# Optimization experiments

Hardware: AMD Instinct MI355X
Metric: run time of the kernel (lower is better)

## Reference

```python
import jax, jax.numpy as jnp
import numpy as np

B, L, D, H = 4, 1024, 1024, 16
HD = D // H
SCALE = 1.0 / np.sqrt(HD)
NOISE_PROB = 0.05
NOISE_SCALE = 0.1


def _linear(x, w, b):
    # torch nn.Linear convention: y = x @ W^T + b, W: [out, in]
    return x @ w.T + b


def _quantum_noise(key, real, imag, p=NOISE_PROB, s=NOISE_SCALE):
    """Phase flips, amplitude noise, and measurement dropout on a complex
    tensor represented as (real, imag). Deterministic given `key`."""
    k_phase, k_amp, k_nr, k_ni, k_meas = jax.random.split(key, 5)
    shape = real.shape
    flip = jnp.where(jax.random.uniform(k_phase, shape) < p, -1.0, 1.0)
    amp_mask = (jax.random.uniform(k_amp, shape) < p).astype(real.dtype)
    new_r = real * flip + jax.random.normal(k_nr, shape, real.dtype) * s * amp_mask
    new_i = imag * flip + jax.random.normal(k_ni, shape, imag.dtype) * s * amp_mask
    keep = 1.0 - (jax.random.uniform(k_meas, shape) < p * 0.5).astype(real.dtype)
    return new_r * keep, new_i * keep


def _heads(t):
    # [B, L, D] -> [B, H, L, HD]
    b, l, _ = t.shape
    return t.reshape(b, l, H, HD).transpose(0, 2, 1, 3)


def setup_inputs() -> dict:
    key = jax.random.key(0)
    ks = jax.random.split(key, 16)
    inp = {
        "x_real": jax.random.normal(ks[0], (B, L, D), jnp.float32),
        "x_imag": jax.random.normal(ks[1], (B, L, D), jnp.float32),
        "mask": jnp.ones((B, L), jnp.int32),
    }
    names = ["qr", "qi", "kr", "ki", "vr", "vi", "or", "oi"]
    for i, n in enumerate(names):
        inp[n + "_w"] = jax.random.normal(ks[2 + i], (D, D), jnp.float32) * 0.02
        inp[n + "_b"] = jnp.zeros((D,), jnp.float32)
    ent = jnp.eye(H) + (jax.random.normal(ks[10], (H, H)) * 0.1) * (
        jax.random.uniform(ks[11], (H, H)) < 0.2
    ).astype(jnp.float32)
    inp["ent"] = ent
    return inp


def reference(x_real, x_imag, mask, qr_w, qr_b, qi_w, qi_b, kr_w, kr_b,
              ki_w, ki_b, vr_w, vr_b, vi_w, vi_b, or_w, or_b, oi_w, oi_b, ent):
    # complex Q/K/V: real part from x.real, imag part from x.imag
    q_r, q_i = _linear(x_real, qr_w, qr_b), _linear(x_imag, qi_w, qi_b)
    k_r, k_i = _linear(x_real, kr_w, kr_b), _linear(x_imag, ki_w, ki_b)
    v_r, v_i = _linear(x_real, vr_w, vr_b), _linear(x_imag, vi_w, vi_b)

    nkey = jax.random.key(1)
    q_r, q_i = _quantum_noise(jax.random.fold_in(nkey, 0), q_r, q_i)
    k_r, k_i = _quantum_noise(jax.random.fold_in(nkey, 1), k_r, k_i)
    v_r, v_i = _quantum_noise(jax.random.fold_in(nkey, 2), v_r, v_i)

    q_r, q_i, k_r, k_i, v_r, v_i = map(_heads, (q_r, q_i, k_r, k_i, v_r, v_i))

    # torch.einsum('bhld,hh->bhld') == per-head scaling by diag(ent)
    d = jnp.diagonal(ent)[None, :, None, None]
    q_r, q_i = q_r * d, q_i * d
    k_r, k_i = k_r * d, k_i * d

    # Re(q . conj(k)) interference score: [B, H, Lq, Lk]
    scores = (jnp.einsum("bhqd,bhkd->bhqk", q_r, k_r)
              + jnp.einsum("bhqd,bhkd->bhqk", q_i, k_i)) * SCALE
    scores = jnp.where(mask[:, None, None, :] == 0, -1e9, scores)
    attn = jax.nn.softmax(scores, axis=-1)

    out_r = jnp.einsum("bhqk,bhkd->bhqd", attn, v_r)
    out_i = jnp.einsum("bhqk,bhkd->bhqd", attn, v_i)
    out_r = out_r.transpose(0, 2, 1, 3).reshape(x_real.shape)
    out_i = out_i.transpose(0, 2, 1, 3).reshape(x_real.shape)

    out_real = _linear(out_r, or_w, or_b)
    out_imag = _linear(out_i, oi_w, oi_b)
    return out_real, out_imag, attn
```

## Files before the change

### kernel.cpp

```cpp
#include <hip/hip_runtime.h>
#include <cstdint>

#define PARTITIONABLE 1

static constexpr int Bsz = 4, Lsz = 1024, Dsz = 1024, Hn = 16, HDsz = 64;
static constexpr size_t ELEMS = (size_t)Bsz * Lsz * Dsz;
static constexpr uint32_t HALF_N = (uint32_t)(ELEMS / 2);
static constexpr float SCALE = 0.125f;
static constexpr float P_NOISE = 0.05f;
static constexpr float S_NOISE = 0.1f;

typedef __attribute__((ext_vector_type(8))) short short8v;
typedef __attribute__((ext_vector_type(4))) float floatx4;
typedef __attribute__((ext_vector_type(4))) unsigned int uint4v;

__host__ __device__ __forceinline__ void tf2x32(uint32_t k0, uint32_t k1,
                                                uint32_t x0, uint32_t x1,
                                                uint32_t& o0, uint32_t& o1) {
  uint32_t ks2 = k0 ^ k1 ^ 0x1BD11BDAu;
  x0 += k0; x1 += k1;
#define TFR(r) { x0 += x1; x1 = (x1 << (r)) | (x1 >> (32 - (r))); x1 ^= x0; }
  TFR(13) TFR(15) TFR(26) TFR(6)
  x0 += k1; x1 += ks2 + 1u;
  TFR(17) TFR(29) TFR(16) TFR(24)
  x0 += ks2; x1 += k0 + 2u;
  TFR(13) TFR(15) TFR(26) TFR(6)
  x0 += k0; x1 += k1 + 3u;
  TFR(17) TFR(29) TFR(16) TFR(24)
  x0 += k1; x1 += ks2 + 4u;
  TFR(13) TFR(15) TFR(26) TFR(6)
  x0 += ks2; x1 += k0 + 5u;
#undef TFR
  o0 = x0; o1 = x1;
}

struct KeySet { uint32_t k[5][2]; };
struct AllKeys { KeySet t[3]; };

__device__ __forceinline__ uint32_t draw_bits(uint32_t k0, uint32_t k1, uint32_t idx) {
#if PARTITIONABLE
  uint32_t o0, o1; tf2x32(k0, k1, 0u, idx, o0, o1);
  return o0 ^ o1;
#else
  uint32_t o0, o1;
  if (idx < HALF_N) { tf2x32(k0, k1, idx, idx + HALF_N, o0, o1); return o0; }
  tf2x32(k0, k1, idx - HALF_N, idx, o0, o1); return o1;
#endif
}

__device__ __forceinline__ float unif01(uint32_t bits) {
  return __uint_as_float((bits >> 9) | 0x3f800000u) - 1.0f;
}

__device__ __forceinline__ float normal_from_bits(uint32_t bits) {
  const float LO = -0.99999994f;
  float f = unif01(bits);
  float x = fmaxf(LO, f * 2.0f + LO);
  float w = -log1pf(-x * x);
  float p;
  if (w < 5.0f) {
    w = w - 2.5f;
    p = 2.81022636e-08f;
    p = fmaf(p, w, 3.43273939e-07f);
    p = fmaf(p, w, -3.5233877e-06f);
    p = fmaf(p, w, -4.39150654e-06f);
    p = fmaf(p, w, 0.00021858087f);
    p = fmaf(p, w, -0.00125372503f);
    p = fmaf(p, w, -0.00417768164f);
    p = fmaf(p, w, 0.246640727f);
    p = fmaf(p, w, 1.50140941f);
  } else {
    w = sqrtf(w) - 3.0f;
    p = -0.000200214257f;
    p = fmaf(p, w, 0.000100950558f);
    p = fmaf(p, w, 0.00134934322f);
    p = fmaf(p, w, -0.00367342844f);
    p = fmaf(p, w, 0.00573950773f);
    p = fmaf(p, w, -0.0076224613f);
    p = fmaf(p, w, 0.00943887047f);
    p = fmaf(p, w, 1.00167406f);
    p = fmaf(p, w, 2.83297682f);
  }
  return 1.41421356f * (p * x);
}

__device__ __forceinline__ uint32_t bf16_rn(float f) {
  uint32_t u = __float_as_uint(f);
  return (u + 0x7FFFu + ((u >> 16) & 1u)) >> 16;
}
__device__ __forceinline__ void cvt_split(float4 v, uint64_t& hi, uint64_t& lo) {
  uint32_t h0 = bf16_rn(v.x), h1 = bf16_rn(v.y), h2 = bf16_rn(v.z), h3 = bf16_rn(v.w);
  float r0 = v.x - __uint_as_float(h0 << 16);
  float r1 = v.y - __uint_as_float(h1 << 16);
  float r2 = v.z - __uint_as_float(h2 << 16);
  float r3 = v.w - __uint_as_float(h3 << 16);
  uint32_t l0 = bf16_rn(r0), l1 = bf16_rn(r1), l2 = bf16_rn(r2), l3 = bf16_rn(r3);
  hi = (uint64_t)h0 | ((uint64_t)h1 << 16) | ((uint64_t)h2 << 32) | ((uint64_t)h3 << 48);
  lo = (uint64_t)l0 | ((uint64_t)l1 << 16) | ((uint64_t)l2 << 32) | ((uint64_t)l3 << 48);
}

struct GemmBatch { const float* X[6]; const float* W[6]; const float* Bv[6]; float* Y[6]; };

__global__ __launch_bounds__(256, 2) void gemm_mfma_kernel(GemmBatch jobs) {
  const int jz = blockIdx.z;
  const float* __restrict__ X = jobs.X[jz];
  const float* __restrict__ W = jobs.W[jz];
  const float* __restrict__ bias = jobs.Bv[jz];
  float* __restrict__ Y = jobs.Y[jz];
  const int n0 = blockIdx.x * 128, m0 = blockIdx.y * 128;

  __shared__ short Ahi[8192], Alo[8192], Bhi[8192], Blo[8192];

  const int tid = (int)threadIdx.x;
  const int q = tid >> 4, kq = tid & 15;
  const int c_st = kq >> 3, m2 = (kq >> 1) & 3, half = kq & 1;
  const int p_st = (q + 16 * m2) ^ m2 ^ (c_st << 2);
  const int stBase = c_st * 4096 + p_st * 8 + half * 4;

  const int l = tid & 63, wid = tid >> 6;
  const int wm = wid >> 1, wn = wid & 1;

  floatx4 acc[4][4];
#pragma unroll
  for (int i = 0; i < 4; ++i)
#pragma unroll
    for (int j = 0; j < 4; ++j) acc[i][j] = (floatx4){0.f, 0.f, 0.f, 0.f};

  const float* xrow = X + (size_t)(m0 + q) * Dsz + kq * 4;
  const float* wrow = W + (size_t)(n0 + q) * Dsz + kq * 4;

  for (int k0 = 0; k0 < Dsz; k0 += 64) {
    __syncthreads();
#pragma unroll
    for (int rr = 0; rr < 8; ++rr) {
      float4 xa = *(const float4*)(xrow + (size_t)rr * 16 * Dsz + k0);
      float4 wb = *(const float4*)(wrow + (size_t)rr * 16 * Dsz + k0);
      uint64_t ah, al, bh, bl;
      cvt_split(xa, ah, al);
      cvt_split(wb, bh, bl);
      const int off = stBase + rr * 512;
      *(uint64_t*)&Ahi[off] = ah; *(uint64_t*)&Alo[off] = al;
      *(uint64_t*)&Bhi[off] = bh; *(uint64_t*)&Blo[off] = bl;
    }
    __syncthreads();
#pragma unroll
    for (int c = 0; c < 2; ++c) {
      const int pr = (l ^ (l >> 4) ^ (c << 2)) & 63;
      short8v aH[4], aL[4], bH[4], bL[4];
#pragma unroll
      for (int t = 0; t < 4; ++t) {
        const int ia = ((c * 8 + wm * 4 + t) * 64 + pr) * 8;
        aH[t] = *(short8v*)&Ahi[ia]; aL[t] = *(short8v*)&Alo[ia];
        const int ib = ((c * 8 + wn * 4 + t) * 64 + pr) * 8;
        bH[t] = *(short8v*)&Bhi[ib]; bL[t] = *(short8v*)&Blo[ib];
      }
#pragma unroll
      for (int mt = 0; mt < 4; ++mt)
#pragma unroll
        for (int nt = 0; nt < 4; ++nt) {
          acc[mt][nt] = __builtin_amdgcn_mfma_f32_16x16x32_bf16(aH[mt], bH[nt], acc[mt][nt], 0, 0, 0);
          acc[mt][nt] = __builtin_amdgcn_mfma_f32_16x16x32_bf16(aH[mt], bL[nt], acc[mt][nt], 0, 0, 0);
          acc[mt][nt] = __builtin_amdgcn_mfma_f32_16x16x32_bf16(aL[mt], bH[nt], acc[mt][nt], 0, 0, 0);
        }
    }
  }
  const int colLane = l & 15, rquad = l >> 4;
#pragma unroll
  for (int nt = 0; nt < 4; ++nt) {
    const int col = n0 + wn * 64 + nt * 16 + colLane;
    const float bv = bias[col];
#pragma unroll
    for (int mt = 0; mt < 4; ++mt) {
      const int r0 = m0 + wm * 64 + mt * 16 + rquad * 4;
#pragma unroll
      for (int j = 0; j < 4; ++j)
        Y[(size_t)(r0 + j) * Dsz + col] = acc[mt][nt][j] + bv;
    }
  }
}

__global__ __launch_bounds__(256, 2) void scores_mfma_kernel(
    const float* __restrict__ qr, const float* __restrict__ qi,
    const float* __restrict__ kr, const float* __restrict__ ki,
    const int* __restrict__ mask, float* __restrict__ attn) {
  const int bh = (int)blockIdx.z;
  const int b = bh >> 4, h = bh & 15;
  const int n0 = blockIdx.x * 128, m0 = blockIdx.y * 128;

  __shared__ short Ahi[8192], Alo[8192], Bhi[8192], Blo[8192];

  const int tid = (int)threadIdx.x;
  const int q = tid >> 4, kq = tid & 15;
  const int c_st = kq >> 3, m2 = (kq >> 1) & 3, half = kq & 1;
  const int p_st = (q + 16 * m2) ^ m2 ^ (c_st << 2);
  const int stBase = c_st * 4096 + p_st * 8 + half * 4;

  const int l = tid & 63, wid = tid >> 6;
  const int wm = wid >> 1, wn = wid & 1;

  floatx4 acc[4][4];
#pragma unroll
  for (int i = 0; i < 4; ++i)
#pragma unroll
    for (int j = 0; j < 4; ++j) acc[i][j] = (floatx4){0.f, 0.f, 0.f, 0.f};

  const size_t qbase = ((size_t)(b * Lsz) + m0 + q) * Dsz + h * HDsz + kq * 4;
  const size_t kbase = ((size_t)(b * Lsz) + n0 + q) * Dsz + h * HDsz + kq * 4;

#pragma unroll
  for (int k0 = 0; k0 < 128; k0 += 64) {
    const float* Xb = k0 ? qi : qr;
    const float* Wb = k0 ? ki : kr;
    __syncthreads();
#pragma unroll
    for (int rr = 0; rr < 8; ++rr) {
      float4 xa = *(const float4*)(Xb + qbase + (size_t)rr * 16 * Dsz);
      float4 wb = *(const float4*)(Wb + kbase + (size_t)rr * 16 * Dsz);
      uint64_t ah, al, bhv, blv;
      cvt_split(xa, ah, al);
      cvt_split(wb, bhv, blv);
      const int off = stBase + rr * 512;
      *(uint64_t*)&Ahi[off] = ah; *(uint64_t*)&Alo[off] = al;
      *(uint64_t*)&Bhi[off] = bhv; *(uint64_t*)&Blo[off] = blv;
    }
    __syncthreads();
#pragma unroll
    for (int c = 0; c < 2; ++c) {
      const int pr = (l ^ (l >> 4) ^ (c << 2)) & 63;
      short8v aH[4], aL[4], bH[4], bL[4];
#pragma unroll
      for (int t = 0; t < 4; ++t) {
        const int ia = ((c * 8 + wm * 4 + t) * 64 + pr) * 8;
        aH[t] = *(short8v*)&Ahi[ia]; aL[t] = *(short8v*)&Alo[ia];
        const int ib = ((c * 8 + wn * 4 + t) * 64 + pr) * 8;
        bH[t] = *(short8v*)&Bhi[ib]; bL[t] = *(short8v*)&Blo[ib];
      }
#pragma unroll
      for (int mt = 0; mt < 4; ++mt)
#pragma unroll
        for (int nt = 0; nt < 4; ++nt) {
          acc[mt][nt] = __builtin_amdgcn_mfma_f32_16x16x32_bf16(aH[mt], bH[nt], acc[mt][nt], 0, 0, 0);
          acc[mt][nt] = __builtin_amdgcn_mfma_f32_16x16x32_bf16(aH[mt], bL[nt], acc[mt][nt], 0, 0, 0);
          acc[mt][nt] = __builtin_amdgcn_mfma_f32_16x16x32_bf16(aL[mt], bH[nt], acc[mt][nt], 0, 0, 0);
        }
    }
  }
  const int colLane = l & 15, rquad = l >> 4;
#pragma unroll
  for (int nt = 0; nt < 4; ++nt) {
    const int col = n0 + wn * 64 + nt * 16 + colLane;
    const int mv = mask[b * Lsz + col];
#pragma unroll
    for (int mt = 0; mt < 4; ++mt) {
      const int r0 = m0 + wm * 64 + mt * 16 + rquad * 4;
#pragma unroll
      for (int j = 0; j < 4; ++j)
        attn[((size_t)bh * Lsz + r0 + j) * Lsz + col] =
            (mv == 0) ? -1e9f : acc[mt][nt][j] * SCALE;
    }
  }
}

__global__ __launch_bounds__(256) void vtrans_kernel(
    const float* __restrict__ vr, const float* __restrict__ vi,
    unsigned short* __restrict__ vth, unsigned short* __restrict__ vtl) {
  const int bh = (int)blockIdx.y;
  const int b = bh >> 4, h = bh & 15;
  const int k0 = blockIdx.x * 64;
  __shared__ uint32_t T[128 * 65];
  const int t = (int)threadIdx.x;
  const int krow = t >> 4, d4 = (t & 15) * 4;

#pragma unroll
  for (int src = 0; src < 2; ++src) {
    const float* V = src ? vi : vr;
    const int nb = src * 64;
#pragma unroll
    for (int p = 0; p < 4; ++p) {
      const int k = p * 16 + krow;
      float4 v = *(const float4*)&V[((size_t)(b * Lsz) + k0 + k) * Dsz + h * HDsz + d4];
      float fv[4] = {v.x, v.y, v.z, v.w};
#pragma unroll
      for (int e = 0; e < 4; ++e) {
        uint32_t hi = bf16_rn(fv[e]);
        float r = fv[e] - __uint_as_float(hi << 16);
        uint32_t lo = bf16_rn(r);
        T[(nb + d4 + e) * 65 + k] = lo | (hi << 16);
      }
    }
  }
  __syncthreads();
  const int n = t >> 1, hf = t & 1;
  const size_t rowb = ((size_t)bh * 128 + n) * Lsz + k0 + hf * 32;
#pragma unroll
  for (int g = 0; g < 4; ++g) {
    uint32_t w[8];
#pragma unroll
    for (int u = 0; u < 8; ++u) w[u] = T[n * 65 + hf * 32 + g * 8 + u];
    uint4v hv, lv;
    hv.x = (w[0] >> 16) | (w[1] & 0xFFFF0000u);
    hv.y = (w[2] >> 16) | (w[3] & 0xFFFF0000u);
    hv.z = (w[4] >> 16) | (w[5] & 0xFFFF0000u);
    hv.w = (w[6] >> 16) | (w[7] & 0xFFFF0000u);
    lv.x = (w[0] & 0xFFFFu) | (w[1] << 16);
    lv.y = (w[2] & 0xFFFFu) | (w[3] << 16);
    lv.z = (w[4] & 0xFFFFu) | (w[5] << 16);
    lv.w = (w[6] & 0xFFFFu) | (w[7] << 16);
    *(uint4v*)&vth[rowb + g * 8] = hv;
    *(uint4v*)&vtl[rowb + g * 8] = lv;
  }
}

__global__ __launch_bounds__(256, 2) void pv_mfma_kernel(
    const float* __restrict__ attn,
    const unsigned short* __restrict__ vth, const unsigned short* __restrict__ vtl,
    float* __restrict__ or_, float* __restrict__ oi_) {
  const int bh = (int)blockIdx.y;
  const int b = bh >> 4, h = bh & 15;
  const int m0 = blockIdx.x * 128;

  __shared__ short Ahi[8192], Alo[8192], Bhi[8192], Blo[8192];

  const int tid = (int)threadIdx.x;
  const int q = tid >> 4, kq = tid & 15;
  const int c_st = kq >> 3, m2 = (kq >> 1) & 3, half = kq & 1;
  const int p_st = (q + 16 * m2) ^ m2 ^ (c_st << 2);
  const int stBase = c_st * 4096 + p_st * 8 + half * 4;

  const int l = tid & 63, wid = tid >> 6;
  const int wm = wid >> 1, wn = wid & 1;

  floatx4 acc[4][4];
#pragma unroll
  for (int i = 0; i < 4; ++i)
#pragma unroll
    for (int j = 0; j < 4; ++j) acc[i][j] = (floatx4){0.f, 0.f, 0.f, 0.f};

  const float* arow = attn + ((size_t)bh * Lsz + m0 + q) * Lsz + kq * 4;
  const unsigned short* bhrow = vth + ((size_t)bh * 128 + q) * Lsz + kq * 4;
  const unsigned short* blrow = vtl + ((size_t)bh * 128 + q) * Lsz + kq * 4;

  for (int k0 = 0; k0 < Lsz; k0 += 64) {
    __syncthreads();
#pragma unroll
    for (int rr = 0; rr < 8; ++rr) {
      float4 av = *(const float4*)(arow + (size_t)rr * 16 * Lsz + k0);
      uint64_t ah, al;
      cvt_split(av, ah, al);
      uint64_t bhv = *(const uint64_t*)(bhrow + (size_t)rr * 16 * Lsz + k0);
      uint64_t blv = *(const uint64_t*)(blrow + (size_t)rr * 16 * Lsz + k0);
      const int off = stBase + rr * 512;
      *(uint64_t*)&Ahi[off] = ah; *(uint64_t*)&Alo[off] = al;
      *(uint64_t*)&Bhi[off] = bhv; *(uint64_t*)&Blo[off] = blv;
    }
    __syncthreads();
#pragma unroll
    for (int c = 0; c < 2; ++c) {
      const int pr = (l ^ (l >> 4) ^ (c << 2)) & 63;
      short8v aH[4], aL[4], bH[4], bL[4];
#pragma unroll
      for (int t = 0; t < 4; ++t) {
        const int ia = ((c * 8 + wm * 4 + t) * 64 + pr) * 8;
        aH[t] = *(short8v*)&Ahi[ia]; aL[t] = *(short8v*)&Alo[ia];
        const int ib = ((c * 8 + wn * 4 + t) * 64 + pr) * 8;
        bH[t] = *(short8v*)&Bhi[ib]; bL[t] = *(short8v*)&Blo[ib];
      }
#pragma unroll
      for (int mt = 0; mt < 4; ++mt)
#pragma unroll
        for (int nt = 0; nt < 4; ++nt) {
          acc[mt][nt] = __builtin_amdgcn_mfma_f32_16x16x32_bf16(aH[mt], bH[nt], acc[mt][nt], 0, 0, 0);
          acc[mt][nt] = __builtin_amdgcn_mfma_f32_16x16x32_bf16(aH[mt], bL[nt], acc[mt][nt], 0, 0, 0);
          acc[mt][nt] = __builtin_amdgcn_mfma_f32_16x16x32_bf16(aL[mt], bH[nt], acc[mt][nt], 0, 0, 0);
        }
    }
  }
  const int colLane = l & 15, rquad = l >> 4;
#pragma unroll
  for (int nt = 0; nt < 4; ++nt) {
    const int col = wn * 64 + nt * 16 + colLane;
    float* O = (col < 64) ? or_ : oi_;
    const int dcol = col & 63;
#pragma unroll
    for (int mt = 0; mt < 4; ++mt) {
      const int r0 = m0 + wm * 64 + mt * 16 + rquad * 4;
#pragma unroll
      for (int j = 0; j < 4; ++j)
        O[((size_t)(b * Lsz) + r0 + j) * Dsz + h * HDsz + dcol] = acc[mt][nt][j];
    }
  }
}

__global__ __launch_bounds__(256) void noise_kernel(
    float* __restrict__ qr, float* __restrict__ qi,
    float* __restrict__ kr, float* __restrict__ ki,
    float* __restrict__ vr, float* __restrict__ vi,
    const float* __restrict__ ent, AllKeys keys) {
  const uint32_t e = blockIdx.x * 256u + threadIdx.x;
  const int j = (int)blockIdx.y;
  float* re; float* im;
  if (j == 0) { re = qr; im = qi; } else if (j == 1) { re = kr; im = ki; }
  else { re = vr; im = vi; }
  const KeySet& ks = keys.t[j];
  const uint32_t b_phase = draw_bits(ks.k[0][0], ks.k[0][1], e);
  const uint32_t b_amp   = draw_bits(ks.k[1][0], ks.k[1][1], e);
  const uint32_t b_nr    = draw_bits(ks.k[2][0], ks.k[2][1], e);
  const uint32_t b_ni    = draw_bits(ks.k[3][0], ks.k[3][1], e);
  const uint32_t b_meas  = draw_bits(ks.k[4][0], ks.k[4][1], e);
  const float flip = (unif01(b_phase) < P_NOISE) ? -1.0f : 1.0f;
  const float amp  = (unif01(b_amp)  < P_NOISE) ? 1.0f : 0.0f;
  const float keep = (unif01(b_meas) < P_NOISE * 0.5f) ? 0.0f : 1.0f;
  const float nr = normal_from_bits(b_nr);
  const float ni = normal_from_bits(b_ni);
  float r  = re[e], iv = im[e];
  r  = (r  * flip + nr * S_NOISE * amp) * keep;
  iv = (iv * flip + ni * S_NOISE * amp) * keep;
  if (j != 2) {
    const int h = ((int)e & (Dsz - 1)) >> 6;
    const float d = ent[h * Hn + h];
    r *= d; iv *= d;
  }
  re[e] = r; im[e] = iv;
}

__global__ __launch_bounds__(256) void softmax_kernel(float* __restrict__ attn) {
  const size_t row = blockIdx.x;
  float* p = attn + row * (size_t)Lsz;
  const int t = (int)threadIdx.x;
  float4 v = ((float4*)p)[t];
  float m = fmaxf(fmaxf(v.x, v.y), fmaxf(v.z, v.w));
  __shared__ float red[4];
  const int lane = t & 63, wv = t >> 6;
#pragma unroll
  for (int off = 32; off; off >>= 1) m = fmaxf(m, __shfl_down(m, off));
  if (lane == 0) red[wv] = m;
  __syncthreads();
  m = fmaxf(fmaxf(red[0], red[1]), fmaxf(red[2], red[3]));
  float e0 = expf(v.x - m), e1 = expf(v.y - m), e2 = expf(v.z - m), e3 = expf(v.w - m);
  float s = (e0 + e1) + (e2 + e3);
  __syncthreads();
#pragma unroll
  for (int off = 32; off; off >>= 1) s += __shfl_down(s, off);
  if (lane == 0) red[wv] = s;
  __syncthreads();
  s = (red[0] + red[1]) + (red[2] + red[3]);
  ((float4*)p)[t] = make_float4(e0 / s, e1 / s, e2 / s, e3 / s);
}

extern "C" void kernel_launch(void* const* d_in, const int* in_sizes, int n_in,
                              void* d_out, int out_size, void* d_ws, size_t ws_size,
                              hipStream_t stream) {
  const float* x_real = (const float*)d_in[0];
  const float* x_imag = (const float*)d_in[1];
  const int*   mask   = (const int*)d_in[2];
  const float* qr_w = (const float*)d_in[3];  const float* qr_b = (const float*)d_in[4];
  const float* qi_w = (const float*)d_in[5];  const float* qi_b = (const float*)d_in[6];
  const float* kr_w = (const float*)d_in[7];  const float* kr_b = (const float*)d_in[8];
  const float* ki_w = (const float*)d_in[9];  const float* ki_b = (const float*)d_in[10];
  const float* vr_w = (const float*)d_in[11]; const float* vr_b = (const float*)d_in[12];
  const float* vi_w = (const float*)d_in[13]; const float* vi_b = (const float*)d_in[14];
  const float* or_w = (const float*)d_in[15]; const float* or_b = (const float*)d_in[16];
  const float* oi_w = (const float*)d_in[17]; const float* oi_b = (const float*)d_in[18];
  const float* ent  = (const float*)d_in[19];

  float* out_real = (float*)d_out;
  float* out_imag = out_real + ELEMS;
  float* attn     = out_imag + ELEMS;

  if (ws_size < 6 * ELEMS * sizeof(float)) return;
  float* ws = (float*)d_ws;
  float* qr = ws + 0 * ELEMS; float* qi = ws + 1 * ELEMS;
  float* kr = ws + 2 * ELEMS; float* ki = ws + 3 * ELEMS;
  float* vr = ws + 4 * ELEMS; float* vi = ws + 5 * ELEMS;
  float* or_tmp = qr;
  float* oi_tmp = qi;
  unsigned short* vth = (unsigned short*)kr;
  unsigned short* vtl = (unsigned short*)ki;

  AllKeys keys;
  for (int j = 0; j < 3; ++j) {
    uint32_t a, b2;
    tf2x32(0u, 1u, 0u, (uint32_t)j, a, b2);
#if PARTITIONABLE
    for (int i = 0; i < 5; ++i)
      tf2x32(a, b2, 0u, (uint32_t)i, keys.t[j].k[i][0], keys.t[j].k[i][1]);
#else
    uint32_t out10[10];
    for (int i = 0; i < 5; ++i) {
      uint32_t o0, o1; tf2x32(a, b2, (uint32_t)i, (uint32_t)(i + 5), o0, o1);
      out10[i] = o0; out10[i + 5] = o1;
    }
    for (int i = 0; i < 5; ++i) { keys.t[j].k[i][0] = out10[2*i]; keys.t[j].k[i][1] = out10[2*i+1]; }
#endif
  }

  GemmBatch pj;
  const float* xs[6] = {x_real, x_imag, x_real, x_imag, x_real, x_imag};
  const float* wsp[6] = {qr_w, qi_w, kr_w, ki_w, vr_w, vi_w};
  const float* bsp[6] = {qr_b, qi_b, kr_b, ki_b, vr_b, vi_b};
  float* ysp[6] = {qr, qi, kr, ki, vr, vi};
  for (int i = 0; i < 6; ++i) { pj.X[i] = xs[i]; pj.W[i] = wsp[i]; pj.Bv[i] = bsp[i]; pj.Y[i] = ysp[i]; }
  gemm_mfma_kernel<<<dim3(8, 32, 6), 256, 0, stream>>>(pj);

  noise_kernel<<<dim3((uint32_t)(ELEMS / 256), 3), 256, 0, stream>>>(qr, qi, kr, ki, vr, vi, ent, keys);

  scores_mfma_kernel<<<dim3(8, 8, 64), 256, 0, stream>>>(qr, qi, kr, ki, mask, attn);

  vtrans_kernel<<<dim3(16, 64), 256, 0, stream>>>(vr, vi, vth, vtl);

  softmax_kernel<<<dim3(Bsz * Hn * Lsz), 256, 0, stream>>>(attn);

  pv_mfma_kernel<<<dim3(8, 64), 256, 0, stream>>>(attn, vth, vtl, or_tmp, oi_tmp);

  GemmBatch oj;
  for (int i = 0; i < 6; ++i) { oj.X[i] = nullptr; oj.W[i] = nullptr; oj.Bv[i] = nullptr; oj.Y[i] = nullptr; }
  oj.X[0] = or_tmp; oj.W[0] = or_w; oj.Bv[0] = or_b; oj.Y[0] = out_real;
  oj.X[1] = oi_tmp; oj.W[1] = oi_w; oj.Bv[1] = oi_b; oj.Y[1] = out_imag;
  gemm_mfma_kernel<<<dim3(8, 32, 2), 256, 0, stream>>>(oj);
}
```

Before: 752.8 us.

## Store intermediates as pre-split bf16 hi/lo and fuse softmax normalization into PV

Inputs and projection weights are now split once into bf16 hi/lo planes by a dedicated kernel. The GEMMs stream those planes straight into LDS with global_load_lds, and Q/K/V/O intermediates are written as hi/lo bf16 instead of fp32. Softmax is replaced by a row-statistics kernel, and the PV kernel computes the exp and normalization itself, writing the final attention values as it builds its A operand. This removes repeated fp32 loads and per-tile conversion work, plus one full read-write pass over the attention matrix. The price is extra split kernels and heavy aliasing of the workspace and output buffers as scratch.

Result: slower. 796.8 us (+5.9%).

```diff
diff --git a/kernel.cpp b/kernel.cpp
--- a/kernel.cpp
+++ b/kernel.cpp
@@ -9,10 +9,19 @@
 static constexpr float SCALE = 0.125f;
 static constexpr float P_NOISE = 0.05f;
 static constexpr float S_NOISE = 0.1f;
-
+static constexpr size_t MBy = 1024 * 1024;
+
+typedef unsigned short u16;
+typedef uint64_t u64;
 typedef __attribute__((ext_vector_type(8))) short short8v;
 typedef __attribute__((ext_vector_type(4))) float floatx4;
 typedef __attribute__((ext_vector_type(4))) unsigned int uint4v;
+
+__device__ __forceinline__ void gload16(const u16* g, u16* l) {
+  __builtin_amdgcn_global_load_lds(
+      (const __attribute__((address_space(1))) void*)(g),
+      (__attribute__((address_space(3))) void*)(l), 16, 0, 0);
+}
 
 __host__ __device__ __forceinline__ void tf2x32(uint32_t k0, uint32_t k1,
                                                 uint32_t x0, uint32_t x1,
@@ -88,37 +97,70 @@
   uint32_t u = __float_as_uint(f);
   return (u + 0x7FFFu + ((u >> 16) & 1u)) >> 16;
 }
-__device__ __forceinline__ void cvt_split(float4 v, uint64_t& hi, uint64_t& lo) {
+__device__ __forceinline__ float bf2f(uint32_t h) { return __uint_as_float(h << 16); }
+__device__ __forceinline__ void cvt_split(float4 v, u64& hi, u64& lo) {
   uint32_t h0 = bf16_rn(v.x), h1 = bf16_rn(v.y), h2 = bf16_rn(v.z), h3 = bf16_rn(v.w);
-  float r0 = v.x - __uint_as_float(h0 << 16);
-  float r1 = v.y - __uint_as_float(h1 << 16);
-  float r2 = v.z - __uint_as_float(h2 << 16);
-  float r3 = v.w - __uint_as_float(h3 << 16);
+  float r0 = v.x - bf2f(h0), r1 = v.y - bf2f(h1), r2 = v.z - bf2f(h2), r3 = v.w - bf2f(h3);
   uint32_t l0 = bf16_rn(r0), l1 = bf16_rn(r1), l2 = bf16_rn(r2), l3 = bf16_rn(r3);
-  hi = (uint64_t)h0 | ((uint64_t)h1 << 16) | ((uint64_t)h2 << 32) | ((uint64_t)h3 << 48);
-  lo = (uint64_t)l0 | ((uint64_t)l1 << 16) | ((uint64_t)l2 << 32) | ((uint64_t)l3 << 48);
-}
-
-struct GemmBatch { const float* X[6]; const float* W[6]; const float* Bv[6]; float* Y[6]; };
-
-__global__ __launch_bounds__(256, 2) void gemm_mfma_kernel(GemmBatch jobs) {
-  const int jz = blockIdx.z;
-  const float* __restrict__ X = jobs.X[jz];
-  const float* __restrict__ W = jobs.W[jz];
-  const float* __restrict__ bias = jobs.Bv[jz];
-  float* __restrict__ Y = jobs.Y[jz];
+  hi = (u64)h0 | ((u64)h1 << 16) | ((u64)h2 << 32) | ((u64)h3 << 48);
+  lo = (u64)l0 | ((u64)l1 << 16) | ((u64)l2 << 32) | ((u64)l3 << 48);
+}
+
+__device__ __forceinline__ void mfma_tile(const u16* Ahs, const u16* Als,
+                                          const u16* Bhs, const u16* Bls,
+                                          int l, int wm, int wn, floatx4 acc[4][4]) {
+#pragma unroll
+  for (int c = 0; c < 2; ++c) {
+    const int pr = (l ^ (l >> 4) ^ (c << 2)) & 63;
+    short8v aH[4], aL[4], bH[4], bL[4];
+#pragma unroll
+    for (int t = 0; t < 4; ++t) {
+      const int ia = ((c * 8 + wm * 4 + t) * 64 + pr) * 8;
+      aH[t] = *(const short8v*)&Ahs[ia]; aL[t] = *(const short8v*)&Als[ia];
+      const int ib = ((c * 8 + wn * 4 + t) * 64 + pr) * 8;
+      bH[t] = *(const short8v*)&Bhs[ib]; bL[t] = *(const short8v*)&Bls[ib];
+    }
+#pragma unroll
+    for (int mt = 0; mt < 4; ++mt)
+#pragma unroll
+      for (int nt = 0; nt < 4; ++nt) {
+        acc[mt][nt] = __builtin_amdgcn_mfma_f32_16x16x32_bf16(aH[mt], bH[nt], acc[mt][nt], 0, 0, 0);
+        acc[mt][nt] = __builtin_amdgcn_mfma_f32_16x16x32_bf16(aH[mt], bL[nt], acc[mt][nt], 0, 0, 0);
+        acc[mt][nt] = __builtin_amdgcn_mfma_f32_16x16x32_bf16(aL[mt], bH[nt], acc[mt][nt], 0, 0, 0);
+      }
+  }
+}
+
+__global__ __launch_bounds__(256) void split_kernel(const float* __restrict__ src,
+                                                    u16* __restrict__ dh,
+                                                    u16* __restrict__ dl, int n4) {
+  int i = blockIdx.x * 256 + (int)threadIdx.x;
+  if (i >= n4) return;
+  float4 v = ((const float4*)src)[i];
+  u64 h, l; cvt_split(v, h, l);
+  ((u64*)dh)[i] = h; ((u64*)dl)[i] = l;
+}
+
+struct GJob { const u16* Ah; const u16* Al; const u16* Wh; const u16* Wl;
+              const float* Wf; const float* bias; float* Yf; u16* Yh; u16* Yl; };
+struct GJobs { GJob j[6]; };
+
+template<int MODE>
+__global__ __launch_bounds__(256, 2) void gemm_kernel(GJobs jobs) {
+  const GJob J = jobs.j[blockIdx.z];
   const int n0 = blockIdx.x * 128, m0 = blockIdx.y * 128;
-
-  __shared__ short Ahi[8192], Alo[8192], Bhi[8192], Blo[8192];
-
+  __shared__ u16 Ahs[8192], Als[8192], Bhs[8192], Bls[8192];
   const int tid = (int)threadIdx.x;
-  const int q = tid >> 4, kq = tid & 15;
-  const int c_st = kq >> 3, m2 = (kq >> 1) & 3, half = kq & 1;
-  const int p_st = (q + 16 * m2) ^ m2 ^ (c_st << 2);
+  const int q_st = tid >> 4, kq = tid & 15;
+  const int c_st = kq >> 3, m2s = (kq >> 1) & 3, half = kq & 1;
+  const int p_st = (q_st + 16 * m2s) ^ m2s ^ (c_st << 2);
   const int stBase = c_st * 4096 + p_st * 8 + half * 4;
-
-  const int l = tid & 63, wid = tid >> 6;
-  const int wm = wid >> 1, wn = wid & 1;
+  const int w = tid >> 6, l = tid & 63;
+  const int cA = w >> 1, m2A = l >> 4;
+  const int qA = (l ^ m2A ^ (cA << 2)) & 15;
+  const int colA = cA * 32 + m2A * 8;
+  const int tb = (w & 1) * 4;
+  const int wm = w >> 1, wn = w & 1;
 
   floatx4 acc[4][4];
 #pragma unroll
@@ -126,281 +168,71 @@
 #pragma unroll
     for (int j = 0; j < 4; ++j) acc[i][j] = (floatx4){0.f, 0.f, 0.f, 0.f};
 
-  const float* xrow = X + (size_t)(m0 + q) * Dsz + kq * 4;
-  const float* wrow = W + (size_t)(n0 + q) * Dsz + kq * 4;
+  const u16* ahp = J.Ah + (size_t)(m0 + qA) * Dsz + colA;
+  const u16* alp = J.Al + (size_t)(m0 + qA) * Dsz + colA;
+  const u16* whp = (MODE == 0) ? J.Wh + (size_t)(n0 + qA) * Dsz + colA : nullptr;
+  const u16* wlp = (MODE == 0) ? J.Wl + (size_t)(n0 + qA) * Dsz + colA : nullptr;
+  const float* wrow = (MODE == 1) ? J.Wf + (size_t)(n0 + q_st) * Dsz + kq * 4 : nullptr;
 
   for (int k0 = 0; k0 < Dsz; k0 += 64) {
     __syncthreads();
 #pragma unroll
-    for (int rr = 0; rr < 8; ++rr) {
-      float4 xa = *(const float4*)(xrow + (size_t)rr * 16 * Dsz + k0);
-      float4 wb = *(const float4*)(wrow + (size_t)rr * 16 * Dsz + k0);
-      uint64_t ah, al, bh, bl;
-      cvt_split(xa, ah, al);
-      cvt_split(wb, bh, bl);
-      const int off = stBase + rr * 512;
-      *(uint64_t*)&Ahi[off] = ah; *(uint64_t*)&Alo[off] = al;
-      *(uint64_t*)&Bhi[off] = bh; *(uint64_t*)&Blo[off] = bl;
+    for (int i = 0; i < 4; ++i) {
+      const size_t go = (size_t)((tb + i) * 16) * Dsz + k0;
+      gload16(ahp + go, &Ahs[(w * 4 + i) * 512]);
+      gload16(alp + go, &Als[(w * 4 + i) * 512]);
+      if (MODE == 0) {
+        gload16(whp + go, &Bhs[(w * 4 + i) * 512]);
+        gload16(wlp + go, &Bls[(w * 4 + i) * 512]);
+      }
+    }
+    if (MODE == 1) {
+#pragma unroll
+      for (int rr = 0; rr < 8; ++rr) {
+        float4 wb = *(const float4*)(wrow + (size_t)rr * 16 * Dsz + k0);
+        u64 bh, bl; cvt_split(wb, bh, bl);
+        const int off = stBase + rr * 512;
+        *(u64*)&Bhs[off] = bh; *(u64*)&Bls[off] = bl;
+      }
     }
     __syncthreads();
-#pragma unroll
-    for (int c = 0; c < 2; ++c) {
-      const int pr = (l ^ (l >> 4) ^ (c << 2)) & 63;
-      short8v aH[4], aL[4], bH[4], bL[4];
-#pragma unroll
-      for (int t = 0; t < 4; ++t) {
-        const int ia = ((c * 8 + wm * 4 + t) * 64 + pr) * 8;
-        aH[t] = *(short8v*)&Ahi[ia]; aL[t] = *(short8v*)&Alo[ia];
-        const int ib = ((c * 8 + wn * 4 + t) * 64 + pr) * 8;
-        bH[t] = *(short8v*)&Bhi[ib]; bL[t] = *(short8v*)&Blo[ib];
-      }
-#pragma unroll
-      for (int mt = 0; mt < 4; ++mt)
-#pragma unroll
-        for (int nt = 0; nt < 4; ++nt) {
-          acc[mt][nt] = __builtin_amdgcn_mfma_f32_16x16x32_bf16(aH[mt], bH[nt], acc[mt][nt], 0, 0, 0);
-          acc[mt][nt] = __builtin_amdgcn_mfma_f32_16x16x32_bf16(aH[mt], bL[nt], acc[mt][nt], 0, 0, 0);
-          acc[mt][nt] = __builtin_amdgcn_mfma_f32_16x16x32_bf16(aL[mt], bH[nt], acc[mt][nt], 0, 0, 0);
-        }
-    }
+    mfma_tile(Ahs, Als, Bhs, Bls, l, wm, wn, acc);
   }
   const int colLane = l & 15, rquad = l >> 4;
 #pragma unroll
   for (int nt = 0; nt < 4; ++nt) {
     const int col = n0 + wn * 64 + nt * 16 + colLane;
-    const float bv = bias[col];
+    const float bv = J.bias[col];
 #pragma unroll
     for (int mt = 0; mt < 4; ++mt) {
       const int r0 = m0 + wm * 64 + mt * 16 + rquad * 4;
 #pragma unroll
-      for (int j = 0; j < 4; ++j)
-        Y[(size_t)(r0 + j) * Dsz + col] = acc[mt][nt][j] + bv;
-    }
-  }
-}
-
-__global__ __launch_bounds__(256, 2) void scores_mfma_kernel(
-    const float* __restrict__ qr, const float* __restrict__ qi,
-    const float* __restrict__ kr, const float* __restrict__ ki,
-    const int* __restrict__ mask, float* __restrict__ attn) {
-  const int bh = (int)blockIdx.z;
-  const int b = bh >> 4, h = bh & 15;
-  const int n0 = blockIdx.x * 128, m0 = blockIdx.y * 128;
-
-  __shared__ short Ahi[8192], Alo[8192], Bhi[8192], Blo[8192];
-
-  const int tid = (int)threadIdx.x;
-  const int q = tid >> 4, kq = tid & 15;
-  const int c_st = kq >> 3, m2 = (kq >> 1) & 3, half = kq & 1;
-  const int p_st = (q + 16 * m2) ^ m2 ^ (c_st << 2);
-  const int stBase = c_st * 4096 + p_st * 8 + half * 4;
-
-  const int l = tid & 63, wid = tid >> 6;
-  const int wm = wid >> 1, wn = wid & 1;
-
-  floatx4 acc[4][4];
-#pragma unroll
-  for (int i = 0; i < 4; ++i)
-#pragma unroll
-    for (int j = 0; j < 4; ++j) acc[i][j] = (floatx4){0.f, 0.f, 0.f, 0.f};
-
-  const size_t qbase = ((size_t)(b * Lsz) + m0 + q) * Dsz + h * HDsz + kq * 4;
-  const size_t kbase = ((size_t)(b * Lsz) + n0 + q) * Dsz + h * HDsz + kq * 4;
-
-#pragma unroll
-  for (int k0 = 0; k0 < 128; k0 += 64) {
-    const float* Xb = k0 ? qi : qr;
-    const float* Wb = k0 ? ki : kr;
-    __syncthreads();
-#pragma unroll
-    for (int rr = 0; rr < 8; ++rr) {
-      float4 xa = *(const float4*)(Xb + qbase + (size_t)rr * 16 * Dsz);
-      float4 wb = *(const float4*)(Wb + kbase + (size_t)rr * 16 * Dsz);
-      uint64_t ah, al, bhv, blv;
-      cvt_split(xa, ah, al);
-      cvt_split(wb, bhv, blv);
-      const int off = stBase + rr * 512;
-      *(uint64_t*)&Ahi[off] = ah; *(uint64_t*)&Alo[off] = al;
-      *(uint64_t*)&Bhi[off] = bhv; *(uint64_t*)&Blo[off] = blv;
-    }
-    __syncthreads();
-#pragma unroll
-    for (int c = 0; c < 2; ++c) {
-      const int pr = (l ^ (l >> 4) ^ (c << 2)) & 63;
-      short8v aH[4], aL[4], bH[4], bL[4];
-#pragma unroll
-      for (int t = 0; t < 4; ++t) {
-        const int ia = ((c * 8 + wm * 4 + t) * 64 + pr) * 8;
-        aH[t] = *(short8v*)&Ahi[ia]; aL[t] = *(short8v*)&Alo[ia];
-        const int ib = ((c * 8 + wn * 4 + t) * 64 + pr) * 8;
-        bH[t] = *(short8v*)&Bhi[ib]; bL[t] = *(short8v*)&Blo[ib];
+      for (int j = 0; j < 4; ++j) {
+        float v = acc[mt][nt][j] + bv;
+        if (MODE == 1) {
+          J.Yf[(size_t)(r0 + j) * Dsz + col] = v;
+        } else {
+          uint32_t hi = bf16_rn(v);
+          uint32_t lo = bf16_rn(v - bf2f(hi));
+          J.Yh[(size_t)(r0 + j) * Dsz + col] = (u16)hi;
+          J.Yl[(size_t)(r0 + j) * Dsz + col] = (u16)lo;
+        }
       }
-#pragma unroll
-      for (int mt = 0; mt < 4; ++mt)
-#pragma unroll
-        for (int nt = 0; nt < 4; ++nt) {
-          acc[mt][nt] = __builtin_amdgcn_mfma_f32_16x16x32_bf16(aH[mt], bH[nt], acc[mt][nt], 0, 0, 0);
-          acc[mt][nt] = __builtin_amdgcn_mfma_f32_16x16x32_bf16(aH[mt], bL[nt], acc[mt][nt], 0, 0, 0);
-          acc[mt][nt] = __builtin_amdgcn_mfma_f32_16x16x32_bf16(aL[mt], bH[nt], acc[mt][nt], 0, 0, 0);
-        }
-    }
-  }
-  const int colLane = l & 15, rquad = l >> 4;
-#pragma unroll
-  for (int nt = 0; nt < 4; ++nt) {
-    const int col = n0 + wn * 64 + nt * 16 + colLane;
-    const int mv = mask[b * Lsz + col];
-#pragma unroll
-    for (int mt = 0; mt < 4; ++mt) {
-      const int r0 = m0 + wm * 64 + mt * 16 + rquad * 4;
-#pragma unroll
-      for (int j = 0; j < 4; ++j)
-        attn[((size_t)bh * Lsz + r0 + j) * Lsz + col] =
-            (mv == 0) ? -1e9f : acc[mt][nt][j] * SCALE;
-    }
-  }
-}
-
-__global__ __launch_bounds__(256) void vtrans_kernel(
-    const float* __restrict__ vr, const float* __restrict__ vi,
-    unsigned short* __restrict__ vth, unsigned short* __restrict__ vtl) {
-  const int bh = (int)blockIdx.y;
-  const int b = bh >> 4, h = bh & 15;
-  const int k0 = blockIdx.x * 64;
-  __shared__ uint32_t T[128 * 65];
-  const int t = (int)threadIdx.x;
-  const int krow = t >> 4, d4 = (t & 15) * 4;
-
-#pragma unroll
-  for (int src = 0; src < 2; ++src) {
-    const float* V = src ? vi : vr;
-    const int nb = src * 64;
-#pragma unroll
-    for (int p = 0; p < 4; ++p) {
-      const int k = p * 16 + krow;
-      float4 v = *(const float4*)&V[((size_t)(b * Lsz) + k0 + k) * Dsz + h * HDsz + d4];
-      float fv[4] = {v.x, v.y, v.z, v.w};
-#pragma unroll
-      for (int e = 0; e < 4; ++e) {
-        uint32_t hi = bf16_rn(fv[e]);
-        float r = fv[e] - __uint_as_float(hi << 16);
-        uint32_t lo = bf16_rn(r);
-        T[(nb + d4 + e) * 65 + k] = lo | (hi << 16);
-      }
-    }
-  }
-  __syncthreads();
-  const int n = t >> 1, hf = t & 1;
-  const size_t rowb = ((size_t)bh * 128 + n) * Lsz + k0 + hf * 32;
-#pragma unroll
-  for (int g = 0; g < 4; ++g) {
-    uint32_t w[8];
-#pragma unroll
-    for (int u = 0; u < 8; ++u) w[u] = T[n * 65 + hf * 32 + g * 8 + u];
-    uint4v hv, lv;
-    hv.x = (w[0] >> 16) | (w[1] & 0xFFFF0000u);
-    hv.y = (w[2] >> 16) | (w[3] & 0xFFFF0000u);
-    hv.z = (w[4] >> 16) | (w[5] & 0xFFFF0000u);
-    hv.w = (w[6] >> 16) | (w[7] & 0xFFFF0000u);
-    lv.x = (w[0] & 0xFFFFu) | (w[1] << 16);
-    lv.y = (w[2] & 0xFFFFu) | (w[3] << 16);
-    lv.z = (w[4] & 0xFFFFu) | (w[5] << 16);
-    lv.w = (w[6] & 0xFFFFu) | (w[7] << 16);
-    *(uint4v*)&vth[rowb + g * 8] = hv;
-    *(uint4v*)&vtl[rowb + g * 8] = lv;
-  }
-}
-
-__global__ __launch_bounds__(256, 2) void pv_mfma_kernel(
-    const float* __restrict__ attn,
-    const unsigned short* __restrict__ vth, const unsigned short* __restrict__ vtl,
-    float* __restrict__ or_, float* __restrict__ oi_) {
-  const int bh = (int)blockIdx.y;
-  const int b = bh >> 4, h = bh & 15;
-  const int m0 = blockIdx.x * 128;
-
-  __shared__ short Ahi[8192], Alo[8192], Bhi[8192], Blo[8192];
-
-  const int tid = (int)threadIdx.x;
-  const int q = tid >> 4, kq = tid & 15;
-  const int c_st = kq >> 3, m2 = (kq >> 1) & 3, half = kq & 1;
-  const int p_st = (q + 16 * m2) ^ m2 ^ (c_st << 2);
-  const int stBase = c_st * 4096 + p_st * 8 + half * 4;
-
-  const int l = tid & 63, wid = tid >> 6;
-  const int wm = wid >> 1, wn = wid & 1;
-
-  floatx4 acc[4][4];
-#pragma unroll
-  for (int i = 0; i < 4; ++i)
-#pragma unroll
-    for (int j = 0; j < 4; ++j) acc[i][j] = (floatx4){0.f, 0.f, 0.f, 0.f};
-
-  const float* arow = attn + ((size_t)bh * Lsz + m0 + q) * Lsz + kq * 4;
-  const unsigned short* bhrow = vth + ((size_t)bh * 128 + q) * Lsz + kq * 4;
-  const unsigned short* blrow = vtl + ((size_t)bh * 128 + q) * Lsz + kq * 4;
-
-  for (int k0 = 0; k0 < Lsz; k0 += 64) {
-    __syncthreads();
-#pragma unroll
-    for (int rr = 0; rr < 8; ++rr) {
-      float4 av = *(const float4*)(arow + (size_t)rr * 16 * Lsz + k0);
-      uint64_t ah, al;
-      cvt_split(av, ah, al);
-      uint64_t bhv = *(const uint64_t*)(bhrow + (size_t)rr * 16 * Lsz + k0);
-      uint64_t blv = *(const uint64_t*)(blrow + (size_t)rr * 16 * Lsz + k0);
-      const int off = stBase + rr * 512;
-      *(uint64_t*)&Ahi[off] = ah; *(uint64_t*)&Alo[off] = al;
-      *(uint64_t*)&Bhi[off] = bhv; *(uint64_t*)&Blo[off] = blv;
-    }
-    __syncthreads();
-#pragma unroll
-    for (int c = 0; c < 2; ++c) {
-      const int pr = (l ^ (l >> 4) ^ (c << 2)) & 63;
-      short8v aH[4], aL[4], bH[4], bL[4];
-#pragma unroll
-      for (int t = 0; t < 4; ++t) {
-        const int ia = ((c * 8 + wm * 4 + t) * 64 + pr) * 8;
-        aH[t] = *(short8v*)&Ahi[ia]; aL[t] = *(short8v*)&Alo[ia];
-        const int ib = ((c * 8 + wn * 4 + t) * 64 + pr) * 8;
-        bH[t] = *(short8v*)&Bhi[ib]; bL[t] = *(short8v*)&Blo[ib];
-      }
-#pragma unroll
-      for (int mt = 0; mt < 4; ++mt)
-#pragma unroll
-        for (int nt = 0; nt < 4; ++nt) {
-          acc[mt][nt] = __builtin_amdgcn_mfma_f32_16x16x32_bf16(aH[mt], bH[nt], acc[mt][nt], 0, 0, 0);
-          acc[mt][nt] = __builtin_amdgcn_mfma_f32_16x16x32_bf16(aH[mt], bL[nt], acc[mt][nt], 0, 0, 0);
-          acc[mt][nt] = __builtin_amdgcn_mfma_f32_16x16x32_bf16(aL[mt], bH[nt], acc[mt][nt], 0, 0, 0);
-        }
-    }
-  }
-  const int colLane = l & 15, rquad = l >> 4;
-#pragma unroll
-  for (int nt = 0; nt < 4; ++nt) {
-    const int col = wn * 64 + nt * 16 + colLane;
-    float* O = (col < 64) ? or_ : oi_;
-    const int dcol = col & 63;
-#pragma unroll
-    for (int mt = 0; mt < 4; ++mt) {
-      const int r0 = m0 + wm * 64 + mt * 16 + rquad * 4;
-#pragma unroll
-      for (int j = 0; j < 4; ++j)
-        O[((size_t)(b * Lsz) + r0 + j) * Dsz + h * HDsz + dcol] = acc[mt][nt][j];
     }
   }
 }
 
 __global__ __launch_bounds__(256) void noise_kernel(
-    float* __restrict__ qr, float* __restrict__ qi,
-    float* __restrict__ kr, float* __restrict__ ki,
-    float* __restrict__ vr, float* __restrict__ vi,
+    u16* __restrict__ qhr, u16* __restrict__ qlr, u16* __restrict__ qhi, u16* __restrict__ qli,
+    u16* __restrict__ khr, u16* __restrict__ klr, u16* __restrict__ khi, u16* __restrict__ kli,
+    u16* __restrict__ vhr, u16* __restrict__ vlr, u16* __restrict__ vhi, u16* __restrict__ vli,
     const float* __restrict__ ent, AllKeys keys) {
   const uint32_t e = blockIdx.x * 256u + threadIdx.x;
   const int j = (int)blockIdx.y;
-  float* re; float* im;
-  if (j == 0) { re = qr; im = qi; } else if (j == 1) { re = kr; im = ki; }
-  else { re = vr; im = vi; }
+  u16 *rh, *rl, *ih, *il;
+  if (j == 0) { rh = qhr; rl = qlr; ih = qhi; il = qli; }
+  else if (j == 1) { rh = khr; rl = klr; ih = khi; il = kli; }
+  else { rh = vhr; rl = vlr; ih = vhi; il = vli; }
   const KeySet& ks = keys.t[j];
   const uint32_t b_phase = draw_bits(ks.k[0][0], ks.k[0][1], e);
   const uint32_t b_amp   = draw_bits(ks.k[1][0], ks.k[1][1], e);
@@ -412,7 +244,8 @@
   const float keep = (unif01(b_meas) < P_NOISE * 0.5f) ? 0.0f : 1.0f;
   const float nr = normal_from_bits(b_nr);
   const float ni = normal_from_bits(b_ni);
-  float r  = re[e], iv = im[e];
+  float r  = bf2f(rh[e]) + bf2f(rl[e]);
+  float iv = bf2f(ih[e]) + bf2f(il[e]);
   r  = (r  * flip + nr * S_NOISE * amp) * keep;
   iv = (iv * flip + ni * S_NOISE * amp) * keep;
   if (j != 2) {
@@ -420,31 +253,227 @@
     const float d = ent[h * Hn + h];
     r *= d; iv *= d;
   }
-  re[e] = r; im[e] = iv;
-}
-
-__global__ __launch_bounds__(256) void softmax_kernel(float* __restrict__ attn) {
-  const size_t row = blockIdx.x;
-  float* p = attn + row * (size_t)Lsz;
+  uint32_t hr = bf16_rn(r);  rh[e] = (u16)hr; rl[e] = (u16)bf16_rn(r - bf2f(hr));
+  uint32_t hi2 = bf16_rn(iv); ih[e] = (u16)hi2; il[e] = (u16)bf16_rn(iv - bf2f(hi2));
+}
+
+__global__ __launch_bounds__(256, 2) void scores_kernel(
+    const u16* __restrict__ qhr, const u16* __restrict__ qlr,
+    const u16* __restrict__ qhi, const u16* __restrict__ qli,
+    const u16* __restrict__ khr, const u16* __restrict__ klr,
+    const u16* __restrict__ khi, const u16* __restrict__ kli,
+    const int* __restrict__ mask, float* __restrict__ attn) {
+  const int bh = (int)blockIdx.z;
+  const int b = bh >> 4, h = bh & 15;
+  const int n0 = blockIdx.x * 128, m0 = blockIdx.y * 128;
+  __shared__ u16 Ahs[8192], Als[8192], Bhs[8192], Bls[8192];
+  const int tid = (int)threadIdx.x;
+  const int w = tid >> 6, l = tid & 63;
+  const int cA = w >> 1, m2A = l >> 4;
+  const int qA = (l ^ m2A ^ (cA << 2)) & 15;
+  const int colA = cA * 32 + m2A * 8;
+  const int tb = (w & 1) * 4;
+  const int wm = w >> 1, wn = w & 1;
+
+  floatx4 acc[4][4];
+#pragma unroll
+  for (int i = 0; i < 4; ++i)
+#pragma unroll
+    for (int j = 0; j < 4; ++j) acc[i][j] = (floatx4){0.f, 0.f, 0.f, 0.f};
+
+  const size_t abase = ((size_t)(b * Lsz) + m0 + qA) * Dsz + h * HDsz + colA;
+  const size_t bbase = ((size_t)(b * Lsz) + n0 + qA) * Dsz + h * HDsz + colA;
+
+#pragma unroll
+  for (int s = 0; s < 2; ++s) {
+    const u16* Ah = s ? qhi : qhr; const u16* Al = s ? qli : qlr;
+    const u16* Bh = s ? khi : khr; const u16* Bl = s ? kli : klr;
+    __syncthreads();
+#pragma unroll
+    for (int i = 0; i < 4; ++i) {
+      const size_t go = (size_t)((tb + i) * 16) * Dsz;
+      gload16(Ah + abase + go, &Ahs[(w * 4 + i) * 512]);
+      gload16(Al + abase + go, &Als[(w * 4 + i) * 512]);
+      gload16(Bh + bbase + go, &Bhs[(w * 4 + i) * 512]);
+      gload16(Bl + bbase + go, &Bls[(w * 4 + i) * 512]);
+    }
+    __syncthreads();
+    mfma_tile(Ahs, Als, Bhs, Bls, l, wm, wn, acc);
+  }
+  const int colLane = l & 15, rquad = l >> 4;
+#pragma unroll
+  for (int nt = 0; nt < 4; ++nt) {
+    const int col = n0 + wn * 64 + nt * 16 + colLane;
+    const int mv = mask[b * Lsz + col];
+#pragma unroll
+    for (int mt = 0; mt < 4; ++mt) {
+      const int r0 = m0 + wm * 64 + mt * 16 + rquad * 4;
+#pragma unroll
+      for (int j = 0; j < 4; ++j)
+        attn[((size_t)bh * Lsz + r0 + j) * Lsz + col] =
+            (mv == 0) ? -1e9f : acc[mt][nt][j] * SCALE;
+    }
+  }
+}
+
+__global__ __launch_bounds__(256) void vtrans_kernel(
+    const u16* __restrict__ vhr, const u16* __restrict__ vlr,
+    const u16* __restrict__ vhi, const u16* __restrict__ vli,
+    u16* __restrict__ vth, u16* __restrict__ vtl) {
+  const int bh = (int)blockIdx.y;
+  const int b = bh >> 4, h = bh & 15;
+  const int k0 = blockIdx.x * 64;
+  __shared__ uint32_t T[128 * 65];
   const int t = (int)threadIdx.x;
-  float4 v = ((float4*)p)[t];
-  float m = fmaxf(fmaxf(v.x, v.y), fmaxf(v.z, v.w));
-  __shared__ float red[4];
-  const int lane = t & 63, wv = t >> 6;
-#pragma unroll
-  for (int off = 32; off; off >>= 1) m = fmaxf(m, __shfl_down(m, off));
-  if (lane == 0) red[wv] = m;
+  const int krow = t >> 4, d4 = (t & 15) * 4;
+
+#pragma unroll
+  for (int src = 0; src < 2; ++src) {
+    const u16* VH = src ? vhi : vhr;
+    const u16* VL = src ? vli : vlr;
+    const int nb = src * 64;
+#pragma unroll
+    for (int p = 0; p < 4; ++p) {
+      const int k = p * 16 + krow;
+      const size_t off = ((size_t)(b * Lsz) + k0 + k) * Dsz + h * HDsz + d4;
+      u64 hv = *(const u64*)(VH + off);
+      u64 lv = *(const u64*)(VL + off);
+#pragma unroll
+      for (int e = 0; e < 4; ++e) {
+        uint32_t hi = (uint32_t)((hv >> (16 * e)) & 0xFFFFu);
+        uint32_t lo = (uint32_t)((lv >> (16 * e)) & 0xFFFFu);
+        T[(nb + d4 + e) * 65 + k] = lo | (hi << 16);
+      }
+    }
+  }
   __syncthreads();
-  m = fmaxf(fmaxf(red[0], red[1]), fmaxf(red[2], red[3]));
-  float e0 = expf(v.x - m), e1 = expf(v.y - m), e2 = expf(v.z - m), e3 = expf(v.w - m);
-  float s = (e0 + e1) + (e2 + e3);
-  __syncthreads();
-#pragma unroll
-  for (int off = 32; off; off >>= 1) s += __shfl_down(s, off);
-  if (lane == 0) red[wv] = s;
-  __syncthreads();
-  s = (red[0] + red[1]) + (red[2] + red[3]);
-  ((float4*)p)[t] = make_float4(e0 / s, e1 / s, e2 / s, e3 / s);
+  const int n = t >> 1, hf = t & 1;
+  const size_t rowb = ((size_t)bh * 128 + n) * Lsz + k0 + hf * 32;
+#pragma unroll
+  for (int g = 0; g < 4; ++g) {
+    uint32_t wv[8];
+#pragma unroll
+    for (int u = 0; u < 8; ++u) wv[u] = T[n * 65 + hf * 32 + g * 8 + u];
+    uint4v hvv, lvv;
+    hvv.x = (wv[0] >> 16) | (wv[1] & 0xFFFF0000u);
+    hvv.y = (wv[2] >> 16) | (wv[3] & 0xFFFF0000u);
+    hvv.z = (wv[4] >> 16) | (wv[5] & 0xFFFF0000u);
+    hvv.w = (wv[6] >> 16) | (wv[7] & 0xFFFF0000u);
+    lvv.x = (wv[0] & 0xFFFFu) | (wv[1] << 16);
+    lvv.y = (wv[2] & 0xFFFFu) | (wv[3] << 16);
+    lvv.z = (wv[4] & 0xFFFFu) | (wv[5] << 16);
+    lvv.w = (wv[6] & 0xFFFFu) | (wv[7] << 16);
+    *(uint4v*)&vth[rowb + g * 8] = hvv;
+    *(uint4v*)&vtl[rowb + g * 8] = lvv;
+  }
+}
+
+__global__ __launch_bounds__(256) void rowstat_kernel(const float* __restrict__ S,
+                                                      float* __restrict__ rowm,
+                                                      float* __restrict__ rowsum) {
+  const int wv = (int)threadIdx.x >> 6, lane = (int)threadIdx.x & 63;
+  const size_t row = (size_t)blockIdx.x * 4 + wv;
+  const float* p = S + row * Lsz;
+  float4 v[4];
+#pragma unroll
+  for (int i = 0; i < 4; ++i) v[i] = *(const float4*)(p + i * 256 + lane * 4);
+  float m = -3.402823466e38f;
+#pragma unroll
+  for (int i = 0; i < 4; ++i)
+    m = fmaxf(m, fmaxf(fmaxf(v[i].x, v[i].y), fmaxf(v[i].z, v[i].w)));
+#pragma unroll
+  for (int d = 1; d < 64; d <<= 1) m = fmaxf(m, __shfl_xor(m, d));
+  float s = 0.f;
+#pragma unroll
+  for (int i = 0; i < 4; ++i)
+    s += expf(v[i].x - m) + expf(v[i].y - m) + expf(v[i].z - m) + expf(v[i].w - m);
+#pragma unroll
+  for (int d = 1; d < 64; d <<= 1) s += __shfl_xor(s, d);
+  if (lane == 0) { rowm[row] = m; rowsum[row] = s; }
+}
+
+__global__ __launch_bounds__(256, 2) void pv_kernel(
+    float* __restrict__ attn, const u16* __restrict__ vth, const u16* __restrict__ vtl,
+    const float* __restrict__ rowm, const float* __restrict__ rowsum,
+    u16* __restrict__ ohr, u16* __restrict__ olr,
+    u16* __restrict__ ohi, u16* __restrict__ oli) {
+  const int bh = (int)blockIdx.y;
+  const int b = bh >> 4, h = bh & 15;
+  const int m0 = blockIdx.x * 128;
+  __shared__ u16 Ahs[8192], Als[8192], Bhs[8192], Bls[8192];
+  const int tid = (int)threadIdx.x;
+  const int q_st = tid >> 4, kq = tid & 15;
+  const int c_st = kq >> 3, m2s = (kq >> 1) & 3, half = kq & 1;
+  const int p_st = (q_st + 16 * m2s) ^ m2s ^ (c_st << 2);
+  const int stBase = c_st * 4096 + p_st * 8 + half * 4;
+  const int w = tid >> 6, l = tid & 63;
+  const int cA = w >> 1, m2A = l >> 4;
+  const int qA = (l ^ m2A ^ (cA << 2)) & 15;
+  const int colA = cA * 32 + m2A * 8;
+  const int tb = (w & 1) * 4;
+  const int wm = w >> 1, wn = w & 1;
+
+  float rmv[8], inv[8];
+#pragma unroll
+  for (int rr = 0; rr < 8; ++rr) {
+    const int row = bh * Lsz + m0 + q_st + rr * 16;
+    rmv[rr] = rowm[row]; inv[rr] = 1.0f / rowsum[row];
+  }
+
+  floatx4 acc[4][4];
+#pragma unroll
+  for (int i = 0; i < 4; ++i)
+#pragma unroll
+    for (int j = 0; j < 4; ++j) acc[i][j] = (floatx4){0.f, 0.f, 0.f, 0.f};
+
+  float* arow = attn + ((size_t)bh * Lsz + m0 + q_st) * Lsz + kq * 4;
+  const u16* bhp = vth + ((size_t)bh * 128 + qA) * Lsz + colA;
+  const u16* blp = vtl + ((size_t)bh * 128 + qA) * Lsz + colA;
+
+  for (int k0 = 0; k0 < Lsz; k0 += 64) {
+    __syncthreads();
+#pragma unroll
+    for (int i = 0; i < 4; ++i) {
+      const size_t go = (size_t)((tb + i) * 16) * Lsz + k0;
+      gload16(bhp + go, &Bhs[(w * 4 + i) * 512]);
+      gload16(blp + go, &Bls[(w * 4 + i) * 512]);
+    }
+#pragma unroll
+    for (int rr = 0; rr < 8; ++rr) {
+      float4 s4 = *(const float4*)(arow + (size_t)rr * 16 * Lsz + k0);
+      float4 p4;
+      p4.x = expf(s4.x - rmv[rr]) * inv[rr];
+      p4.y = expf(s4.y - rmv[rr]) * inv[rr];
+      p4.z = expf(s4.z - rmv[rr]) * inv[rr];
+      p4.w = expf(s4.w - rmv[rr]) * inv[rr];
+      *(float4*)(arow + (size_t)rr * 16 * Lsz + k0) = p4;
+      u64 ah, al; cvt_split(p4, ah, al);
+      const int off = stBase + rr * 512;
+      *(u64*)&Ahs[off] = ah; *(u64*)&Als[off] = al;
+    }
+    __syncthreads();
+    mfma_tile(Ahs, Als, Bhs, Bls, l, wm, wn, acc);
+  }
+  const int colLane = l & 15, rquad = l >> 4;
+#pragma unroll
+  for (int nt = 0; nt < 4; ++nt) {
+    const int col = wn * 64 + nt * 16 + colLane;
+    u16* oh = (col < 64) ? ohr : ohi;
+    u16* ol = (col < 64) ? olr : oli;
+    const int dcol = col & 63;
+#pragma unroll
+    for (int mt = 0; mt < 4; ++mt) {
+      const int r0 = m0 + wm * 64 + mt * 16 + rquad * 4;
+#pragma unroll
+      for (int j = 0; j < 4; ++j) {
+        float v = acc[mt][nt][j];
+        uint32_t hi = bf16_rn(v);
+        uint32_t lo = bf16_rn(v - bf2f(hi));
+        const size_t oidx = ((size_t)(b * Lsz) + r0 + j) * Dsz + h * HDsz + dcol;
+        oh[oidx] = (u16)hi; ol[oidx] = (u16)lo;
+      }
+    }
+  }
 }
 
 extern "C" void kernel_launch(void* const* d_in, const int* in_sizes, int n_in,
@@ -453,12 +482,10 @@
   const float* x_real = (const float*)d_in[0];
   const float* x_imag = (const float*)d_in[1];
   const int*   mask   = (const int*)d_in[2];
-  const float* qr_w = (const float*)d_in[3];  const float* qr_b = (const float*)d_in[4];
-  const float* qi_w = (const float*)d_in[5];  const float* qi_b = (const float*)d_in[6];
-  const float* kr_w = (const float*)d_in[7];  const float* kr_b = (const float*)d_in[8];
-  const float* ki_w = (const float*)d_in[9];  const float* ki_b = (const float*)d_in[10];
-  const float* vr_w = (const float*)d_in[11]; const float* vr_b = (const float*)d_in[12];
-  const float* vi_w = (const float*)d_in[13]; const float* vi_b = (const float*)d_in[14];
+  const float* pw[6] = {(const float*)d_in[3], (const float*)d_in[5], (const float*)d_in[7],
+                        (const float*)d_in[9], (const float*)d_in[11], (const float*)d_in[13]};
+  const float* pb[6] = {(const float*)d_in[4], (const float*)d_in[6], (const float*)d_in[8],
+                        (const float*)d_in[10], (const float*)d_in[12], (const float*)d_in[14]};
   const float* or_w = (const float*)d_in[15]; const float* or_b = (const float*)d_in[16];
   const float* oi_w = (const float*)d_in[17]; const float* oi_b = (const float*)d_in[18];
   const float* ent  = (const float*)d_in[19];
@@ -467,15 +494,24 @@
   float* out_imag = out_real + ELEMS;
   float* attn     = out_imag + ELEMS;
 
-  if (ws_size < 6 * ELEMS * sizeof(float)) return;
-  float* ws = (float*)d_ws;
-  float* qr = ws + 0 * ELEMS; float* qi = ws + 1 * ELEMS;
-  float* kr = ws + 2 * ELEMS; float* ki = ws + 3 * ELEMS;
-  float* vr = ws + 4 * ELEMS; float* vi = ws + 5 * ELEMS;
-  float* or_tmp = qr;
-  float* oi_tmp = qi;
-  unsigned short* vth = (unsigned short*)kr;
-  unsigned short* vtl = (unsigned short*)ki;
+  if (ws_size < 96 * MBy) return;
+  uint8_t* wsb = (uint8_t*)d_ws;
+  u16* qhr = (u16*)(wsb + 0 * MBy);  u16* qlr = (u16*)(wsb + 8 * MBy);
+  u16* qhi = (u16*)(wsb + 16 * MBy); u16* qli = (u16*)(wsb + 24 * MBy);
+  u16* khr = (u16*)(wsb + 32 * MBy); u16* klr = (u16*)(wsb + 40 * MBy);
+  u16* khi = (u16*)(wsb + 48 * MBy); u16* kli = (u16*)(wsb + 56 * MBy);
+  u16* xhr = (u16*)(wsb + 64 * MBy); u16* xlr = (u16*)(wsb + 72 * MBy);
+  u16* xhi = (u16*)(wsb + 80 * MBy); u16* xli = (u16*)(wsb + 88 * MBy);
+  u16* vth = (u16*)(wsb + 64 * MBy); u16* vtl = (u16*)(wsb + 80 * MBy);
+  u16* ohr = (u16*)(wsb + 0 * MBy);  u16* olr = (u16*)(wsb + 8 * MBy);
+  u16* ohi = (u16*)(wsb + 16 * MBy); u16* oli = (u16*)(wsb + 24 * MBy);
+
+  uint8_t* atb = (uint8_t*)attn;
+  u16* vhr = (u16*)(atb + 0 * MBy);  u16* vlr = (u16*)(atb + 8 * MBy);
+  u16* vhi = (u16*)(atb + 16 * MBy); u16* vli = (u16*)(atb + 24 * MBy);
+
+  float* rowm = out_real;
+  float* rowsum = out_real + 65536;
 
   AllKeys keys;
   for (int j = 0; j < 3; ++j) {
@@ -494,27 +530,42 @@
 #endif
   }
 
-  GemmBatch pj;
-  const float* xs[6] = {x_real, x_imag, x_real, x_imag, x_real, x_imag};
-  const float* wsp[6] = {qr_w, qi_w, kr_w, ki_w, vr_w, vi_w};
-  const float* bsp[6] = {qr_b, qi_b, kr_b, ki_b, vr_b, vi_b};
-  float* ysp[6] = {qr, qi, kr, ki, vr, vi};
-  for (int i = 0; i < 6; ++i) { pj.X[i] = xs[i]; pj.W[i] = wsp[i]; pj.Bv[i] = bsp[i]; pj.Y[i] = ysp[i]; }
-  gemm_mfma_kernel<<<dim3(8, 32, 6), 256, 0, stream>>>(pj);
-
-  noise_kernel<<<dim3((uint32_t)(ELEMS / 256), 3), 256, 0, stream>>>(qr, qi, kr, ki, vr, vi, ent, keys);
-
-  scores_mfma_kernel<<<dim3(8, 8, 64), 256, 0, stream>>>(qr, qi, kr, ki, mask, attn);
-
-  vtrans_kernel<<<dim3(16, 64), 256, 0, stream>>>(vr, vi, vth, vtl);
-
-  softmax_kernel<<<dim3(Bsz * Hn * Lsz), 256, 0, stream>>>(attn);
-
-  pv_mfma_kernel<<<dim3(8, 64), 256, 0, stream>>>(attn, vth, vtl, or_tmp, oi_tmp);
-
-  GemmBatch oj;
-  for (int i = 0; i < 6; ++i) { oj.X[i] = nullptr; oj.W[i] = nullptr; oj.Bv[i] = nullptr; oj.Y[i] = nullptr; }
-  oj.X[0] = or_tmp; oj.W[0] = or_w; oj.Bv[0] = or_b; oj.Y[0] = out_real;
-  oj.X[1] = oi_tmp; oj.W[1] = oi_w; oj.Bv[1] = oi_b; oj.Y[1] = out_imag;
-  gemm_mfma_kernel<<<dim3(8, 32, 2), 256, 0, stream>>>(oj);
-}
+  split_kernel<<<dim3(4096), 256, 0, stream>>>(x_real, xhr, xlr, (int)(ELEMS / 4));
+  split_kernel<<<dim3(4096), 256, 0, stream>>>(x_imag, xhi, xli, (int)(ELEMS / 4));
+  u16* pwh[6]; u16* pwl[6];
+  for (int z = 0; z < 6; ++z) {
+    pwh[z] = (u16*)(atb + 32 * MBy + (size_t)z * 4 * MBy);
+    pwl[z] = pwh[z] + (size_t)Dsz * Dsz;
+    split_kernel<<<dim3(1024), 256, 0, stream>>>(pw[z], pwh[z], pwl[z], Dsz * Dsz / 4);
+  }
+
+  GJobs pj{};
+  u16* yh[6] = {qhr, qhi, khr, khi, vhr, vhi};
+  u16* yl[6] = {qlr, qli, klr, kli, vlr, vli};
+  const u16* ah6[6] = {xhr, xhi, xhr, xhi, xhr, xhi};
+  const u16* al6[6] = {xlr, xli, xlr, xli, xlr, xli};
+  for (int z = 0; z < 6; ++z) {
+    pj.j[z].Ah = ah6[z]; pj.j[z].Al = al6[z];
+    pj.j[z].Wh = pwh[z]; pj.j[z].Wl = pwl[z]; pj.j[z].Wf = nullptr;
+    pj.j[z].bias = pb[z]; pj.j[z].Yf = nullptr; pj.j[z].Yh = yh[z]; pj.j[z].Yl = yl[z];
+  }
+  gemm_kernel<0><<<dim3(8, 32, 6), 256, 0, stream>>>(pj);
+
+  noise_kernel<<<dim3((uint32_t)(ELEMS / 256), 3), 256, 0, stream>>>(
+      qhr, qlr, qhi, qli, khr, klr, khi, kli, vhr, vlr, vhi, vli, ent, keys);
+
+  vtrans_kernel<<<dim3(16, 64), 256, 0, stream>>>(vhr, vlr, vhi, vli, vth, vtl);
+
+  scores_kernel<<<dim3(8, 8, 64), 256, 0, stream>>>(
+      qhr, qlr, qhi, qli, khr, klr, khi, kli, mask, attn);
+
+  rowstat_kernel<<<dim3(16384), 256, 0, stream>>>(attn, rowm, rowsum);
+
+  pv_kernel<<<dim3(8, 64), 256, 0, stream>>>(attn, vth, vtl, rowm, rowsum,
+                                             ohr, olr, ohi, oli);
+
+  GJobs oj{};
+  oj.j[0].Ah = ohr; oj.j[0].Al = olr; oj.j[0].Wf = or_w; oj.j[0].bias = or_b; oj.j[0].Yf = out_real;
+  oj.j[1].Ah = ohi; oj.j[1].Al = oli; oj.j[1].Wf = oi_w; oj.j[1].bias = oi_b; oj.j[1].Yf = out_imag;
+  gemm_kernel<1><<<dim3(8, 32, 2), 256, 0, stream>>>(oj);
+}
```
